# Optimization experiments

Hardware: AMD Instinct MI355X
Metric: run time of the kernel (lower is better)

## Reference

```python
import jax, jax.numpy as jnp
import numpy as np

B, S, D = 2, 2048, 4096
H, KV, HD = 32, 8, 128
ROPE_BASE = 10000.0


def rotate_half(x):
    x1, x2 = jnp.split(x, 2, axis=-1)
    return jnp.concatenate((-x2, x1), axis=-1)


def rope_tables(seq_len, head_dim, position_ids):
    inv_freq = 1.0 / (ROPE_BASE ** (jnp.arange(0, head_dim, 2, dtype=jnp.float32) / head_dim))
    t = jnp.arange(seq_len, dtype=jnp.float32)
    freqs = t[:, None] * inv_freq[None, :]            # [S, HD/2]
    emb = jnp.concatenate((freqs, freqs), axis=-1)     # [S, HD]
    cos = jnp.cos(emb)[position_ids][:, None]          # [B, 1, S, HD]
    sin = jnp.sin(emb)[position_ids][:, None]
    return cos, sin


def setup_inputs() -> dict:
    key = jax.random.key(0)
    ks = jax.random.split(key, 5)
    sc = 0.02
    return {
        "hidden_states": jax.random.normal(ks[0], (B, S, D), jnp.float32),
        "Wq": jax.random.normal(ks[1], (H * HD, D), jnp.float32) * sc,
        "Wk": jax.random.normal(ks[2], (KV * HD, D), jnp.float32) * sc,
        "Wv": jax.random.normal(ks[3], (KV * HD, D), jnp.float32) * sc,
        "Wo": jax.random.normal(ks[4], (D, H * HD), jnp.float32) * sc,
        "position_ids": jnp.broadcast_to(jnp.arange(S, dtype=jnp.int32), (B, S)),
    }


def reference(hidden_states, Wq, Wk, Wv, Wo, position_ids):
    b, s, _ = hidden_states.shape
    n_rep = H // KV

    q = (hidden_states @ Wq.T).reshape(b, s, H, HD).transpose(0, 2, 1, 3)   # [B,H,S,HD]
    k = (hidden_states @ Wk.T).reshape(b, s, KV, HD).transpose(0, 2, 1, 3)  # [B,KV,S,HD]
    v = (hidden_states @ Wv.T).reshape(b, s, KV, HD).transpose(0, 2, 1, 3)

    cos, sin = rope_tables(s, HD, position_ids)
    q = q * cos + rotate_half(q) * sin
    k = k * cos + rotate_half(k) * sin

    # repeat_kv: [B,KV,S,HD] -> [B,H,S,HD]
    k = jnp.repeat(k, n_rep, axis=1)
    v = jnp.repeat(v, n_rep, axis=1)

    scores = jnp.einsum("bhqd,bhkd->bhqk", q, k) / jnp.sqrt(jnp.float32(HD))
    # causal additive mask (what the surrounding model always supplies)
    causal = jnp.tril(jnp.ones((s, s), dtype=bool))
    scores = jnp.where(causal[None, None], scores, jnp.finfo(jnp.float32).min)
    attn = jax.nn.softmax(scores.astype(jnp.float32), axis=-1).astype(q.dtype)

    out = jnp.einsum("bhqk,bhkd->bhqd", attn, v)        # [B,H,S,HD]
    out = out.transpose(0, 2, 1, 3).reshape(b, s, H * HD)
    return out @ Wo.T
```

## Files before the change

kernel.cpp:

```cpp
#include <hip/hip_runtime.h>
#include <stdint.h>
#include <math.h>

#define B_  2
#define S_  2048
#define D_  4096
#define H_  32
#define KV_ 8
#define HD_ 128
#define M_  (B_ * S_)

typedef unsigned short u16;
typedef unsigned int   u32;

__device__ __forceinline__ float bf2f(u16 u) {
  union { u32 i; float f; } x; x.i = ((u32)u) << 16; return x.f;
}
__device__ __forceinline__ u16 f2bf(float f) {
  union { float f; u32 i; } x; x.f = f;
  u32 r = x.i + 0x7fffu + ((x.i >> 16) & 1u);
  return (u16)(r >> 16);
}
__device__ __forceinline__ u32 pack_bf16_rh(float hi, float lo) {
  union { float f; u32 i; } a, c; a.f = hi; c.f = lo;
  return __builtin_amdgcn_perm(a.i + 0x8000u, c.i + 0x8000u, 0x07060302u);
}

typedef __attribute__((ext_vector_type(8))) short bf16x8;
typedef __attribute__((ext_vector_type(4))) float f32x4;

__device__ __forceinline__ void async_cp16(const void* g, void* l) {
  __builtin_amdgcn_global_load_lds(
      (const __attribute__((address_space(1))) u32*)g,
      (__attribute__((address_space(3))) u32*)l, 16, 0, 0);
}

#define SBAR   asm volatile("s_barrier" ::: "memory")
#define WAITL0 asm volatile("s_waitcnt lgkmcnt(0)" ::: "memory")
#define WAITV(n) asm volatile("s_waitcnt vmcnt(" #n ")" ::: "memory")

__global__ void k_f32_to_bf16(const float* __restrict__ src, u16* __restrict__ dst, int n) {
  int i = (blockIdx.x * 256 + threadIdx.x) * 4;
  if (i >= n) return;
  float4 v = *(const float4*)(src + i);
  ushort4 o;
  o.x = f2bf(v.x); o.y = f2bf(v.y); o.z = f2bf(v.z); o.w = f2bf(v.w);
  *(ushort4*)(dst + i) = o;
}

template <typename OutT>
__global__ __launch_bounds__(512, 2) void k_gemm256_bt(const u16* __restrict__ A,
                                                       const u16* __restrict__ Bm,
                                                       OutT* __restrict__ C,
                                                       int M, int N, int K) {
  __shared__ __align__(16) u16 As[2][256 * 64];
  __shared__ __align__(16) u16 Bs[2][256 * 64];
  const int t = threadIdx.x;
  const int l = t & 63;
  const int w = t >> 6;
  const int wr = w >> 2, wc = w & 3;
  const int quad = l >> 4, lm = l & 15, l7 = l & 7;

  const u32 gx = gridDim.x, gy = gridDim.y;
  const u32 bid = blockIdx.y * gx + blockIdx.x;
  const u32 q8 = (gx * gy) >> 3;
  const u32 cidx = (bid & 7u) * q8 + (bid >> 3);
  const int m0 = (int)(cidx % gy) * 256;
  const int n0 = (int)(cidx / gy) * 256;

  const int srow = t >> 3;
  const int scb  = (t & 7) ^ (srow & 7);
  const u16* srcA = A  + (size_t)(m0 + srow) * K + scb * 8;
  const u16* srcB = Bm + (size_t)(n0 + srow) * K + scb * 8;
  u16* dA = &As[0][0] + t * 8;
  u16* dB = &Bs[0][0] + t * 8;
  const size_t row64 = (size_t)64 * K;

  const int rowA = (wr * 128 + lm) * 64;
  const int rowB = (wc * 64 + lm) * 64;
  const int kq0 = ((0 * 4 + quad) ^ l7) * 8;
  const int kq1 = ((1 * 4 + quad) ^ l7) * 8;
  const u16* As0 = &As[0][0];
  const u16* Bs0 = &Bs[0][0];

  f32x4 acc[8][4];
#pragma unroll
  for (int i2 = 0; i2 < 8; ++i2)
#pragma unroll
    for (int j2 = 0; j2 < 4; ++j2) {
      f32x4 z = {0.f, 0.f, 0.f, 0.f};
      acc[i2][j2] = z;
    }

  auto stgA = [&](int buf, int kt, int h) {
    const u16* s = srcA + (size_t)kt * 64 + (size_t)(h * 128) * K;
    u16* d = dA + buf * 16384 + h * 8192;
    async_cp16(s, d);
    async_cp16(s + row64, d + 4096);
  };
  auto stgB = [&](int buf, int kt, int h) {
    const u16* s = srcB + (size_t)kt * 64 + (size_t)(h * 128) * K;
    u16* d = dB + buf * 16384 + h * 8192;
    async_cp16(s, d);
    async_cp16(s + row64, d + 4096);
  };

  stgA(0, 0, 0); stgA(0, 0, 1);
  stgB(0, 0, 0); stgB(0, 0, 1);
  stgB(1, 1, 0); stgB(1, 1, 1);
  WAITV(4);
  SBAR;

  const int iters = K >> 7;
  for (int i = 0; i < iters; ++i) {
    const int kt = 2 * i;
    const bool notLast = (i + 1 < iters);
#pragma unroll
    for (int hf = 0; hf < 2; ++hf) {
      bf16x8 bfr[4][2];
#pragma unroll
      for (int q = 0; q < 4; ++q) {
        if (q == 0) {
#pragma unroll
          for (int fn = 0; fn < 4; ++fn) {
            const int ro = hf * 16384 + rowB + fn * 1024;
            bfr[fn][0] = *(const bf16x8*)&Bs0[ro + kq0];
            bfr[fn][1] = *(const bf16x8*)&Bs0[ro + kq1];
          }
        }
        bf16x8 af[2][2];
#pragma unroll
        for (int fo = 0; fo < 2; ++fo) {
          const int ro = hf * 16384 + rowA + (2 * q + fo) * 1024;
          af[fo][0] = *(const bf16x8*)&As0[ro + kq0];
          af[fo][1] = *(const bf16x8*)&As0[ro + kq1];
        }
        if (hf == 0) {
          if (q == 0)      stgA(1, kt + 1, 0);
          else if (q == 1) stgA(1, kt + 1, 1);
          else if (q == 2) { if (notLast) stgB(0, kt + 2, 0); }
          else {
            if (notLast) { stgB(0, kt + 2, 1); WAITV(4); }
            else WAITV(0);
          }
        } else if (notLast) {
          if (q == 0)      stgA(0, kt + 2, 0);
          else if (q == 1) stgA(0, kt + 2, 1);
          else if (q == 2) stgB(1, kt + 3, 0);
          else { stgB(1, kt + 3, 1); WAITV(4); }
        }
        SBAR;
        WAITL0;
        __builtin_amdgcn_s_setprio(1);
#pragma unroll
        for (int fo = 0; fo < 2; ++fo)
#pragma unroll
          for (int fn = 0; fn < 4; ++fn)
            acc[2 * q + fo][fn] = __builtin_amdgcn_mfma_f32_16x16x32_bf16(
                af[fo][0], bfr[fn][0], acc[2 * q + fo][fn], 0, 0, 0);
#pragma unroll
        for (int fo = 0; fo < 2; ++fo)
#pragma unroll
          for (int fn = 0; fn < 4; ++fn)
            acc[2 * q + fo][fn] = __builtin_amdgcn_mfma_f32_16x16x32_bf16(
                af[fo][1], bfr[fn][1], acc[2 * q + fo][fn], 0, 0, 0);
        __builtin_amdgcn_s_setprio(0);
        SBAR;
      }
    }
  }

#pragma unroll
  for (int fm = 0; fm < 8; ++fm) {
    const int row = m0 + wr * 128 + fm * 16 + quad * 4;
#pragma unroll
    for (int fn = 0; fn < 4; ++fn) {
      const int col = n0 + wc * 64 + fn * 16 + lm;
#pragma unroll
      for (int r = 0; r < 4; ++r) {
        float v = acc[fm][fn][r];
        if constexpr (sizeof(OutT) == 2)
          C[(size_t)(row + r) * N + col] = (OutT)f2bf(v);
        else
          C[(size_t)(row + r) * N + col] = v;
      }
    }
  }
}

__global__ __launch_bounds__(256) void k_rope(u16* __restrict__ Q, u16* __restrict__ Km,
                                              const int* __restrict__ pos_ids) {
  const int t = threadIdx.x;
  const int bs = blockIdx.x * 4 + (t >> 6);
  const int d = t & 63;
  const int hg = blockIdx.y;
  const float pos = (float)pos_ids[bs];
  const float ang = pos * expf(-(float)d * 0.1439115683121279f);
  float sn, cs;
  sincosf(ang, &sn, &cs);
#pragma unroll
  for (int j = 0; j < 4; j++) {
    const int hh = hg * 4 + j;
    const bool isQ = (hh < H_);
    const float sc = isQ ? 0.12751744661679714f : 1.0f;
    u16* p = isQ ? (Q + (size_t)bs * (H_ * HD_) + hh * HD_)
                 : (Km + (size_t)bs * 2048 + (hh - H_) * HD_);
    const float x1 = bf2f(p[d]);
    const float x2 = bf2f(p[d + 64]);
    p[d]      = f2bf((x1 * cs - x2 * sn) * sc);
    p[d + 64] = f2bf((x2 * cs + x1 * sn) * sc);
  }
}

__global__ __launch_bounds__(256) void k_transpose_v(const u16* __restrict__ KVb,
                                                     u16* __restrict__ Vt) {
  __shared__ u16 tile[64][136];
  const int s0 = blockIdx.x * 64;
  const int kvh = blockIdx.y & 7, b = blockIdx.y >> 3;
  const int t = threadIdx.x;
  const int sl = t >> 2, d0 = (t & 3) * 32;
  const u16* src = KVb + (size_t)(b * S_ + s0 + sl) * 2048 + 1024 + kvh * 128 + d0;
#pragma unroll
  for (int j = 0; j < 4; j++)
    *(uint4*)&tile[sl][d0 + j * 8] = *(const uint4*)(src + j * 8);
  __syncthreads();
  const int lt = t & 63, wv = t >> 6;
  u16* dst = Vt + ((size_t)(b * KV_ + kvh) * HD_) * (size_t)S_ + s0 + lt;
#pragma unroll
  for (int i = 0; i < 32; i++) {
    const int d = i * 4 + wv;
    dst[(size_t)d * S_] = tile[lt][d];
  }
}

__global__ __launch_bounds__(256, 2) void k_attn_mfma(const u16* __restrict__ Q,
                                                      const u16* __restrict__ KVb,
                                                      const u16* __restrict__ Vt,
                                                      u16* __restrict__ O) {
  __shared__ __align__(16) u16 Ks[2][64 * 128];
  __shared__ __align__(16) u16 Vs[2][128 * 64];
  __shared__ __align__(16) u16 Ps[128 * 64];
  const int h = blockIdx.y, b = blockIdx.z;
  const int kvh = h >> 2;
  const int t = threadIdx.x;
  const int w = t >> 6, l = t & 63;
  const int quad = l >> 4, lm = l & 15, l7 = l & 7;
  const int wq = w * 32;

  const u16* kSrc[4]; const u16* vSrc[4];
  int dstOff[4];
#pragma unroll
  for (int j = 0; j < 4; j++) {
    const int c = w * 4 + j;
    kSrc[j] = KVb + (size_t)(b * S_ + c * 4 + (l >> 4)) * 2048 + kvh * 128
              + 8 * ((l & 15) ^ ((c & 1) * 4 + (l >> 4)));
    vSrc[j] = Vt + ((size_t)(b * KV_ + kvh) * HD_ + c * 8 + (l >> 3)) * (size_t)S_
              + 8 * ((l & 7) ^ (l >> 3));
    dstOff[j] = c * 512 + l * 8;
  }

  for (int seg = 0; seg < 2; ++seg) {
    const int qt = seg ? blockIdx.x : (S_ / 128 - 1) - blockIdx.x;
    const int q0 = qt * 128;
    const int nTiles = (qt + 1) * 2;

    bf16x8 qf[2][4];
#pragma unroll
    for (int nt = 0; nt < 2; nt++)
#pragma unroll
      for (int ks = 0; ks < 4; ks++) {
        const int qrow = q0 + wq + nt * 16 + lm;
        qf[nt][ks] = *(const bf16x8*)(Q + (size_t)(b * S_ + qrow) * (H_ * HD_)
                                      + h * HD_ + ks * 32 + quad * 8);
      }

    f32x4 Oa[8][2];
#pragma unroll
    for (int dt = 0; dt < 8; dt++)
#pragma unroll
      for (int nt = 0; nt < 2; nt++) {
        f32x4 z = {0.f, 0.f, 0.f, 0.f};
        Oa[dt][nt] = z;
      }
    float lsum[2] = {0.f, 0.f};

#pragma unroll
    for (int j = 0; j < 4; j++) {
      async_cp16(kSrc[j], &Ks[0][dstOff[j]]);
      async_cp16(vSrc[j], &Vs[0][dstOff[j]]);
    }

    for (int tile = 0; tile < nTiles; tile++) {
      const int cur = tile & 1;
      __builtin_amdgcn_s_waitcnt(0);
      __syncthreads();
      if (tile + 1 < nTiles) {
        const size_t kAdv = (size_t)(tile + 1) * 64 * 2048;
        const int vAdv = (tile + 1) * 64;
        const int nxt = cur ^ 1;
#pragma unroll
        for (int j = 0; j < 4; j++) {
          async_cp16(kSrc[j] + kAdv, &Ks[nxt][dstOff[j]]);
          async_cp16(vSrc[j] + vAdv, &Vs[nxt][dstOff[j]]);
        }
      }
      const u16* KsC = Ks[cur];
      const u16* VsC = Vs[cur];

      f32x4 st[4][2];
#pragma unroll
      for (int kvt = 0; kvt < 4; kvt++)
#pragma unroll
        for (int nt = 0; nt < 2; nt++) {
          f32x4 z = {0.f, 0.f, 0.f, 0.f};
          st[kvt][nt] = z;
        }
#pragma unroll
      for (int ks = 0; ks < 4; ks++) {
        bf16x8 kf[4];
#pragma unroll
        for (int kvt = 0; kvt < 4; kvt++)
          kf[kvt] = *(const bf16x8*)&KsC[(kvt * 16 + lm) * 128 + ((ks * 4 + quad) ^ l7) * 8];
        __builtin_amdgcn_s_setprio(1);
#pragma unroll
        for (int kvt = 0; kvt < 4; kvt++) {
          st[kvt][0] = __builtin_amdgcn_mfma_f32_16x16x32_bf16(kf[kvt], qf[0][ks], st[kvt][0], 0, 0, 0);
          st[kvt][1] = __builtin_amdgcn_mfma_f32_16x16x32_bf16(kf[kvt], qf[1][ks], st[kvt][1], 0, 0, 0);
        }
        __builtin_amdgcn_s_setprio(0);
      }

      const int kt0 = tile * 64;
      const bool diag = (tile >= nTiles - 2);
#pragma unroll
      for (int nt = 0; nt < 2; nt++) {
        const int qg = q0 + wq + nt * 16 + lm;
        const int prow = (wq + nt * 16 + lm) * 64;
#pragma unroll
        for (int kvt = 0; kvt < 4; kvt++) {
          float p[4];
#pragma unroll
          for (int r = 0; r < 4; r++) {
            float e = exp2f(st[kvt][nt][r]);
            if (diag) {
              const int kg = kt0 + kvt * 16 + quad * 4 + r;
              e = (kg <= qg) ? e : 0.f;
            }
            p[r] = e;
            lsum[nt] += e;
          }
          uint2 pk;
          pk.x = pack_bf16_rh(p[1], p[0]);
          pk.y = pack_bf16_rh(p[3], p[2]);
          const int pb = (2 * kvt + (quad >> 1)) ^ l7;
          *(uint2*)&Ps[prow + pb * 8 + (quad & 1) * 4] = pk;
        }
      }

#pragma unroll
      for (int ks2 = 0; ks2 < 2; ks2++) {
        const int pboff = ((ks2 * 4 + quad) ^ l7) * 8;
        bf16x8 pf0 = *(const bf16x8*)&Ps[(wq + lm) * 64 + pboff];
        bf16x8 pf1 = *(const bf16x8*)&Ps[(wq + 16 + lm) * 64 + pboff];
        __builtin_amdgcn_s_setprio(1);
#pragma unroll
        for (int dt = 0; dt < 8; dt++) {
          bf16x8 vf = *(const bf16x8*)&VsC[(dt * 16 + lm) * 64 + pboff];
          Oa[dt][0] = __builtin_amdgcn_mfma_f32_16x16x32_bf16(vf, pf0, Oa[dt][0], 0, 0, 0);
          Oa[dt][1] = __builtin_amdgcn_mfma_f32_16x16x32_bf16(vf, pf1, Oa[dt][1], 0, 0, 0);
        }
        __builtin_amdgcn_s_setprio(0);
      }
    }

#pragma unroll
    for (int nt = 0; nt < 2; nt++) {
      lsum[nt] += __shfl_xor(lsum[nt], 16);
      lsum[nt] += __shfl_xor(lsum[nt], 32);
    }
#pragma unroll
    for (int nt = 0; nt < 2; nt++) {
      const float inv = 1.f / lsum[nt];
      const int qg = q0 + wq + nt * 16 + lm;
      u16* obase = O + (size_t)(b * S_ + qg) * (H_ * HD_) + h * HD_ + quad * 4;
#pragma unroll
      for (int dt = 0; dt < 8; dt++) {
        uint2 pk;
        pk.x = pack_bf16_rh(Oa[dt][nt][1] * inv, Oa[dt][nt][0] * inv);
        pk.y = pack_bf16_rh(Oa[dt][nt][3] * inv, Oa[dt][nt][2] * inv);
        *(uint2*)(obase + dt * 16) = pk;
      }
    }
  }
}

extern "C" void kernel_launch(void* const* d_in, const int* in_sizes, int n_in,
                              void* d_out, int out_size, void* d_ws, size_t ws_size,
                              hipStream_t stream) {
  const float* hs = (const float*)d_in[0];
  const float* Wq = (const float*)d_in[1];
  const float* Wk = (const float*)d_in[2];
  const float* Wv = (const float*)d_in[3];
  const float* Wo = (const float*)d_in[4];
  const int*  pos = (const int*)d_in[5];
  float* out = (float*)d_out;

  u16* hbuf = (u16*)d_ws;
  u16* wbuf = hbuf + (size_t)M_ * D_;
  u16* wkvb = wbuf + (size_t)(H_ * HD_) * D_;
  u16* Qb   = wkvb + (size_t)2048 * D_;
  u16* KVb  = Qb   + (size_t)M_ * (H_ * HD_);
  u16* Vt   = wkvb;

  const int nHid = M_ * D_;
  const int nWq  = H_ * HD_ * D_;
  const int nWk  = KV_ * HD_ * D_;

  k_f32_to_bf16<<<nHid / 1024, 256, 0, stream>>>(hs, hbuf, nHid);
  k_f32_to_bf16<<<nWq  / 1024, 256, 0, stream>>>(Wq, wbuf, nWq);
  k_f32_to_bf16<<<nWk  / 1024, 256, 0, stream>>>(Wk, wkvb, nWk);
  k_f32_to_bf16<<<nWk  / 1024, 256, 0, stream>>>(Wv, wkvb + (size_t)1024 * D_, nWk);

  dim3 blk(512);
  k_gemm256_bt<u16><<<dim3((H_ * HD_) / 256, M_ / 256), blk, 0, stream>>>(hbuf, wbuf, Qb,  M_, H_ * HD_, D_);
  k_gemm256_bt<u16><<<dim3(2048 / 256, M_ / 256),       blk, 0, stream>>>(hbuf, wkvb, KVb, M_, 2048,     D_);

  k_f32_to_bf16<<<nWq / 1024, 256, 0, stream>>>(Wo, wbuf, nWq);

  k_rope<<<dim3(M_ / 4, (H_ + KV_) / 4), 256, 0, stream>>>(Qb, KVb, pos);

  k_transpose_v<<<dim3(S_ / 64, B_ * KV_), 256, 0, stream>>>(KVb, Vt);

  k_attn_mfma<<<dim3(S_ / 256, H_, B_), 256, 0, stream>>>(Qb, KVb, Vt, hbuf);

  k_gemm256_bt<float><<<dim3(D_ / 256, M_ / 256), blk, 0, stream>>>(hbuf, wbuf, out, M_, D_, H_ * HD_);
}
```

Measured before the change: 718.1 us.

## Software-pipeline LDS fragment loads in GEMM with double-buffered A registers

The GEMM main loop now prefetches the next A fragments from LDS into a second register buffer while the MFMAs for the current fragment run. The B fragments for the next half-tile are loaded right after the last MFMA group, and the first fragments are loaded before the loop starts. The explicit lgkmcnt(0) wait is replaced by a scheduling barrier, so the compiler inserts the finer-grained waits itself. This aims to hide LDS read latency behind matrix work, at the cost of more live vector registers and a more fragile ordering against the async global-to-LDS staging and barriers.

Measured after the change: 764.9 us. 1.07x slower.

```diff
diff --git a/kernel.cpp b/kernel.cpp
--- a/kernel.cpp
+++ b/kernel.cpp
@@ -36,8 +36,8 @@
 }
 
 #define SBAR   asm volatile("s_barrier" ::: "memory")
-#define WAITL0 asm volatile("s_waitcnt lgkmcnt(0)" ::: "memory")
 #define WAITV(n) asm volatile("s_waitcnt vmcnt(" #n ")" ::: "memory")
+#define SCHED0 __builtin_amdgcn_sched_barrier(0)
 
 __global__ void k_f32_to_bf16(const float* __restrict__ src, u16* __restrict__ dst, int n) {
   int i = (blockIdx.x * 256 + threadIdx.x) * 4;
@@ -92,6 +92,26 @@
       acc[i2][j2] = z;
     }
 
+  bf16x8 af[2][2][2];
+  bf16x8 bfr[4][2];
+
+  auto loadA = [&](bf16x8 (&dst)[2][2], int hfb, int qn) {
+#pragma unroll
+    for (int fo = 0; fo < 2; ++fo) {
+      const int ro = hfb * 16384 + rowA + (2 * qn + fo) * 1024;
+      dst[fo][0] = *(const bf16x8*)&As0[ro + kq0];
+      dst[fo][1] = *(const bf16x8*)&As0[ro + kq1];
+    }
+  };
+  auto loadB = [&](int hfb) {
+#pragma unroll
+    for (int fn = 0; fn < 4; ++fn) {
+      const int ro = hfb * 16384 + rowB + fn * 1024;
+      bfr[fn][0] = *(const bf16x8*)&Bs0[ro + kq0];
+      bfr[fn][1] = *(const bf16x8*)&Bs0[ro + kq1];
+    }
+  };
+
   auto stgA = [&](int buf, int kt, int h) {
     const u16* s = srcA + (size_t)kt * 64 + (size_t)(h * 128) * K;
     u16* d = dA + buf * 16384 + h * 8192;
@@ -110,6 +130,8 @@
   stgB(1, 1, 0); stgB(1, 1, 1);
   WAITV(4);
   SBAR;
+  loadB(0);
+  loadA(af[0], 0, 0);
 
   const int iters = K >> 7;
   for (int i = 0; i < iters; ++i) {
@@ -117,24 +139,8 @@
     const bool notLast = (i + 1 < iters);
 #pragma unroll
     for (int hf = 0; hf < 2; ++hf) {
-      bf16x8 bfr[4][2];
 #pragma unroll
       for (int q = 0; q < 4; ++q) {
-        if (q == 0) {
-#pragma unroll
-          for (int fn = 0; fn < 4; ++fn) {
-            const int ro = hf * 16384 + rowB + fn * 1024;
-            bfr[fn][0] = *(const bf16x8*)&Bs0[ro + kq0];
-            bfr[fn][1] = *(const bf16x8*)&Bs0[ro + kq1];
-          }
-        }
-        bf16x8 af[2][2];
-#pragma unroll
-        for (int fo = 0; fo < 2; ++fo) {
-          const int ro = hf * 16384 + rowA + (2 * q + fo) * 1024;
-          af[fo][0] = *(const bf16x8*)&As0[ro + kq0];
-          af[fo][1] = *(const bf16x8*)&As0[ro + kq1];
-        }
         if (hf == 0) {
           if (q == 0)      stgA(1, kt + 1, 0);
           else if (q == 1) stgA(1, kt + 1, 1);
@@ -150,21 +156,25 @@
           else { stgB(1, kt + 3, 1); WAITV(4); }
         }
         SBAR;
-        WAITL0;
+        if (q < 3)                       loadA(af[(q + 1) & 1], hf, q + 1);
+        else if (hf == 0 || notLast)     loadA(af[0], hf ^ 1, 0);
+        SCHED0;
+        bf16x8 (&afc)[2][2] = af[q & 1];
         __builtin_amdgcn_s_setprio(1);
 #pragma unroll
         for (int fo = 0; fo < 2; ++fo)
 #pragma unroll
           for (int fn = 0; fn < 4; ++fn)
             acc[2 * q + fo][fn] = __builtin_amdgcn_mfma_f32_16x16x32_bf16(
-                af[fo][0], bfr[fn][0], acc[2 * q + fo][fn], 0, 0, 0);
+                afc[fo][0], bfr[fn][0], acc[2 * q + fo][fn], 0, 0, 0);
 #pragma unroll
         for (int fo = 0; fo < 2; ++fo)
 #pragma unroll
           for (int fn = 0; fn < 4; ++fn)
             acc[2 * q + fo][fn] = __builtin_amdgcn_mfma_f32_16x16x32_bf16(
-                af[fo][1], bfr[fn][1], acc[2 * q + fo][fn], 0, 0, 0);
+                afc[fo][1], bfr[fn][1], acc[2 * q + fo][fn], 0, 0, 0);
         __builtin_amdgcn_s_setprio(0);
+        if (q == 3 && (hf == 0 || notLast)) loadB(hf ^ 1);
         SBAR;
       }
     }
```
